# Kernel tuning notes

Hardware: AMD Instinct MI355X
Metric: run time of the kernel (lower is better)

Reference implementation:

```python
import jax, jax.numpy as jnp
import numpy as np

NF = 128                 # num_filters
C_STATE = NF * 3 // 2    # ODE state channels (output of conv_up_embed_1) = 192
EPS = 1e-5               # InstanceNorm2d eps
N_STEPS = 4              # fixed-step RK4 steps over t in [0, 1]
DT = 1.0 / N_STEPS

nl = jax.nn.softplus     # get_nonlinearity('softplus')


def instance_norm(x):
    # InstanceNorm2d(affine=False): normalize over (H, W) per (N, C)
    m = x.mean(axis=(2, 3), keepdims=True)
    v = x.var(axis=(2, 3), keepdims=True)
    return (x - m) * jax.lax.rsqrt(v + EPS)


def conv2d(x, w, b):
    y = jax.lax.conv_general_dilated(
        x, w, window_strides=(1, 1), padding='SAME',
        dimension_numbers=('NCHW', 'OIHW', 'NCHW'))
    return y + b[None, :, None, None]


def setup_inputs() -> dict:
    key = jax.random.key(0)
    ks = jax.random.split(key, 10)
    B, H, W = 4, 64, 64
    s = 0.05
    return {
        'x':    jax.random.normal(ks[0], (B, NF, H, W), jnp.float32),
        'skip': jax.random.normal(ks[1], (B, NF, 2 * H, 2 * W), jnp.float32),
        # InitialVelocity: 3x3 conv nf -> nf
        'iv_w': jax.random.normal(ks[2], (NF, NF, 3, 3), jnp.float32) * s,
        'iv_b': jax.random.normal(ks[3], (NF,), jnp.float32) * s,
        # conv_up_embed_1: 1x1 conv 3nf -> 3nf//2
        'up_w': jax.random.normal(ks[4], (C_STATE, 3 * NF, 1, 1), jnp.float32) * s,
        'up_b': jax.random.normal(ks[5], (C_STATE,), jnp.float32) * s,
        # ConvSODEFunc convs (second-order: dv/dt = f(z, v))
        'f1_w': jax.random.normal(ks[6], (C_STATE // 2, C_STATE, 3, 3), jnp.float32) * s,
        'f1_b': jax.random.normal(ks[7], (C_STATE // 2,), jnp.float32) * s,
        'f2_w': jax.random.normal(ks[8], (C_STATE // 2, C_STATE // 2, 3, 3), jnp.float32) * s,
        'f2_b': jax.random.normal(ks[9], (C_STATE // 2,), jnp.float32) * s,
    }


def _ode_f(y, f1_w, f1_b, f2_w, f2_b):
    # second-order ODE: state y = [z, v]; dz/dt = v, dv/dt = f(y)
    c = y.shape[1] // 2
    v = y[:, c:]
    u = nl(conv2d(instance_norm(y), f1_w, f1_b))   # [B, C/2, H, W]
    dv = nl(conv2d(instance_norm(u), f2_w, f2_b))  # [B, C/2, H, W]
    return jnp.concatenate([v, dv], axis=1)


def reference(x, skip, iv_w, iv_b, up_w, up_b, f1_w, f1_b, f2_w, f2_b):
    # InitialVelocity (counter == 0): concat learned velocity -> 2*nf channels
    v0 = nl(conv2d(instance_norm(x), iv_w, iv_b))
    y = jnp.concatenate([x, v0], axis=1)                       # [B, 2nf, H, W]
    B, C, H, W = y.shape
    # bilinear upsample x2, align_corners=False (half-pixel centers)
    y = jax.image.resize(y, (B, C, 2 * H, 2 * W), method='bilinear')
    y = jnp.concatenate([y, skip], axis=1)                     # [B, 3nf, 2H, 2W]
    y = nl(conv2d(y, up_w, up_b))                              # [B, 3nf//2, 2H, 2W]
    # ODEBlock: integrate t: 0 -> 1, fixed-step RK4 via lax.scan
    f = lambda s: _ode_f(s, f1_w, f1_b, f2_w, f2_b)

    def step(s, _):
        k1 = f(s)
        k2 = f(s + 0.5 * DT * k1)
        k3 = f(s + 0.5 * DT * k2)
        k4 = f(s + DT * k3)
        s = s + (DT / 6.0) * (k1 + 2.0 * k2 + 2.0 * k3 + k4)
        return s, None

    y, _ = jax.lax.scan(step, y, None, length=N_STEPS)
    return y
```

## Files before the change

### kernel.cpp

```cpp
#include <hip/hip_runtime.h>
#include <math.h>

#define BB 4
#define NF 128
#define CS 192
#define CH 96
#define H1 64
#define W1 64
#define H2 128
#define W2 128
#define P1 (H1*W1)
#define P2 (H2*W2)
#define EPSV 1e-5f
#define DTV 0.25f
#define NSLICE 32
#define SLOTSZ (1536 * NSLICE)

typedef __attribute__((ext_vector_type(8))) short short8;
typedef __attribute__((ext_vector_type(4))) float f32x4;

__device__ __forceinline__ float softplus_f(float x) {
    return fmaxf(x, 0.0f) + __logf(1.0f + __expf(-fabsf(x)));
}
__device__ __forceinline__ unsigned f2bf(float f) {
    unsigned u = __float_as_uint(f);
    return (u + 0x7FFFu + ((u >> 16) & 1u)) >> 16;
}
__device__ __forceinline__ float bf2f(short s) {
    return __uint_as_float(((unsigned)(unsigned short)s) << 16);
}
__device__ __forceinline__ int packbf(float a, float b) {
    return (int)(f2bf(a) | (f2bf(b) << 16));
}

__global__ __launch_bounds__(256) void zero_kernel(float* __restrict__ p, int n) {
    int i = blockIdx.x * 256 + threadIdx.x;
    if (i < n) p[i] = 0.f;
}

__global__ __launch_bounds__(256) void meanvar_raw_kernel(const float* __restrict__ x,
                                                          float* __restrict__ mv, int HW) {
    int bc = blockIdx.x;
    const float* p = x + (size_t)bc * HW;
    float s = 0.f, s2 = 0.f;
    for (int i = threadIdx.x; i < HW; i += 256) {
        float v = p[i];
        s += v; s2 += v * v;
    }
    __shared__ float sh[512];
    sh[threadIdx.x] = s; sh[256 + threadIdx.x] = s2;
    __syncthreads();
    for (int o = 128; o > 0; o >>= 1) {
        if (threadIdx.x < o) {
            sh[threadIdx.x] += sh[threadIdx.x + o];
            sh[256 + threadIdx.x] += sh[256 + threadIdx.x + o];
        }
        __syncthreads();
    }
    if (threadIdx.x == 0) {
        mv[2 * bc]     = sh[0];
        mv[2 * bc + 1] = sh[256];
    }
}

__global__ __launch_bounds__(256) void repack_w_kernel(const float* __restrict__ w,
                                                       short* __restrict__ wq,
                                                       int Cout, int Cin) {
    int idx = blockIdx.x * 256 + threadIdx.x;
    int total = Cout * Cin * 9;
    if (idx >= total) return;
    int tap = idx % 9;
    int t = idx / 9;
    int ci = t % Cin, co = t / Cin;
    int NITl = Cin >> 5, COGl = Cout >> 4;
    int cog = co >> 4, lx = co & 15;
    int it = ci >> 5, q = (ci >> 3) & 3, e = ci & 7;
    size_t o = ((((size_t)tap * NITl + it) * COGl + cog) * 64 + q * 16 + lx) * 8 + e;
    wq[o] = (short)f2bf(w[idx]);
}

__global__ __launch_bounds__(256) void repack_w1_kernel(const float* __restrict__ w,
                                                        short* __restrict__ wq,
                                                        int Cout, int Cin) {
    int idx = blockIdx.x * 256 + threadIdx.x;
    if (idx >= Cout * Cin) return;
    int ci = idx % Cin, co = idx / Cin;
    int COGl = Cout >> 4;
    int cog = co >> 4, lx = co & 15;
    int it = ci >> 5, q = (ci >> 3) & 3, e = ci & 7;
    size_t o = (((size_t)it * COGl + cog) * 64 + q * 16 + lx) * 8 + e;
    wq[o] = (short)f2bf(w[idx]);
}

__global__ __launch_bounds__(256) void xcvt_kernel(const float* __restrict__ x,
                                                   short* __restrict__ xbf) {
    __shared__ int buf[64 * 68];
    const int tid = threadIdx.x;
    const int px = tid & 63, jj = tid >> 6;
    const int px0 = blockIdx.x * 64;
    const int b = blockIdx.y;
#pragma unroll
    for (int ji = 0; ji < 16; ji++) {
        int j = jj + 4 * ji;
        int c = 2 * j;
        float a = x[((size_t)(b * NF + c)) * P1 + px0 + px];
        float d = x[((size_t)(b * NF + c + 1)) * P1 + px0 + px];
        buf[px * 68 + j] = packbf(a, d);
    }
    __syncthreads();
#pragma unroll
    for (int k = 0; k < 4; k++) {
        int idx = tid + 256 * k;
        int p2 = idx >> 4, w4 = idx & 15;
        int4 v = *(const int4*)&buf[p2 * 68 + w4 * 4];
        *(int4*)(xbf + ((size_t)b * P1 + px0 + p2) * NF + w4 * 8) = v;
    }
}

template<int CIN, int NCG, bool OUTBF, bool SUMS>
__global__ __launch_bounds__(256) void conv3x3_mfma(
    const short* __restrict__ in, const float* __restrict__ mvsums,
    const short* __restrict__ wq, const float* __restrict__ bias,
    float* __restrict__ outf, short* __restrict__ outbf, float* __restrict__ osum,
    int CoutT, int H, int W, int outC, int outCoff, int coblk)
{
    constexpr int ROWS = CIN + 8;
    constexpr int STGI = 180 * ROWS / 2;
    constexpr int SMEMI = (OUTBF && 128 * 52 > STGI) ? 128 * 52 : STGI;
    constexpr int NCGH = NCG / 2;
    __shared__ int smem[SMEMI];
    short* xt = (short*)smem;
    __shared__ float mvm[CIN], mvr[CIN];
    __shared__ float shs[2 * CH];
    const int tid = threadIdx.x;
    const int w4 = tid >> 6, lane = tid & 63;
    const int wy = w4 & 1, wc = w4 >> 1;
    const int lx = lane & 15, q = lane >> 4;
    const int x0 = blockIdx.x * 16, y0 = blockIdx.y * 8;
    const int b = blockIdx.z / coblk;
    const int co_base = (blockIdx.z % coblk) * (NCG * 16);
    const int slice = (blockIdx.x + (blockIdx.y << 3)) & (NSLICE - 1);
    const int HWp = H * W;
    const short* inb = in + (size_t)b * HWp * CIN;

    const float invHW = 1.0f / (float)HWp;
    for (int c = tid; c < CIN; c += 256) {
        float s = 0.f, s2 = 0.f;
#pragma unroll
        for (int sl = 0; sl < NSLICE; sl++) {
            s  += mvsums[(size_t)sl * 1536 + (b * CIN + c) * 2];
            s2 += mvsums[(size_t)sl * 1536 + (b * CIN + c) * 2 + 1];
        }
        float m  = s * invHW;
        float var = fmaxf(s2 * invHW - m * m, 0.f);
        mvm[c] = m;
        mvr[c] = rsqrtf(var + EPSV);
    }
    if (SUMS) for (int c = tid; c < 2 * CH; c += 256) shs[c] = 0.f;
    __syncthreads();

    constexpr int PARTS = CIN / 8;
    constexpr int TOT = 180 * PARTS;
    constexpr int NJ = (TOT + 255) / 256;
#pragma unroll
    for (int k = 0; k < NJ; k++) {
        int j = tid + 256 * k;
        if (j < TOT) {
            int px = j / PARTS, part = j - px * PARTS;
            int yy = px / 18, xx = px - yy * 18;
            int gy = y0 + yy - 1, gx = x0 + xx - 1;
            int4 wv = make_int4(0, 0, 0, 0);
            if (gy >= 0 && gy < H && gx >= 0 && gx < W) {
                int cb = part * 8;
                short8 v = *(const short8*)(inb + (size_t)(gy * W + gx) * CIN + cb);
                float4 m0 = *(const float4*)&mvm[cb];
                float4 m1 = *(const float4*)&mvm[cb + 4];
                float4 r0 = *(const float4*)&mvr[cb];
                float4 r1 = *(const float4*)&mvr[cb + 4];
                wv.x = packbf((bf2f(v[0]) - m0.x) * r0.x, (bf2f(v[1]) - m0.y) * r0.y);
                wv.y = packbf((bf2f(v[2]) - m0.z) * r0.z, (bf2f(v[3]) - m0.w) * r0.w);
                wv.z = packbf((bf2f(v[4]) - m1.x) * r1.x, (bf2f(v[5]) - m1.y) * r1.y);
                wv.w = packbf((bf2f(v[6]) - m1.z) * r1.z, (bf2f(v[7]) - m1.w) * r1.w);
            }
            *(int4*)(&xt[px * ROWS + part * 8]) = wv;
        }
    }
    __syncthreads();

    f32x4 acc[4][NCGH];
#pragma unroll
    for (int rr = 0; rr < 4; rr++)
#pragma unroll
        for (int cg = 0; cg < NCGH; cg++) acc[rr][cg] = (f32x4)(0.f);

    constexpr int NIT = CIN / 32;
    constexpr int NC = 9 * NIT;
    const int COGl = CoutT >> 4;
    const short* wbase = wq + ((size_t)((co_base >> 4) + wc * NCGH) * 64 + lane) * 8;

    auto ldw = [&](int c, short8* dst) {
        int it = c / 9, tap = c - 9 * it;
        int slot0 = (tap * NIT + it) * COGl;
#pragma unroll
        for (int cg = 0; cg < NCGH; cg++)
            dst[cg] = *(const short8*)(wbase + (size_t)(slot0 + cg) * 512);
    };
    auto body = [&](int c, const short8* a) {
        int it = c / 9, tap = c - 9 * it;
        int dy = tap / 3, dx = tap - 3 * (tap / 3);
        short8 bfr[4];
#pragma unroll
        for (int rr = 0; rr < 4; rr++)
            bfr[rr] = *(const short8*)(
                &xt[((wy * 4 + rr + dy) * 18 + lx + dx) * ROWS + it * 32 + q * 8]);
#pragma unroll
        for (int rr = 0; rr < 4; rr++)
#pragma unroll
            for (int cg = 0; cg < NCGH; cg++)
                acc[rr][cg] = __builtin_amdgcn_mfma_f32_16x16x32_bf16(
                    a[cg], bfr[rr], acc[rr][cg], 0, 0, 0);
    };

    short8 aA[NCGH], aB[NCGH], aC[NCGH];
    ldw(0, aA);
    if (NC > 1) ldw(1, aB);
    for (int c = 0; c < NC; c += 3) {
        if (c + 2 < NC) ldw(c + 2, aC);
        body(c, aA);
        if (c + 3 < NC) ldw(c + 3, aA);
        if (c + 1 < NC) body(c + 1, aB);
        if (c + 4 < NC) ldw(c + 4, aB);
        if (c + 2 < NC) body(c + 2, aC);
    }

    if (OUTBF) __syncthreads();

    float s1l[NCGH][4], s2l[NCGH][4];
    if (SUMS) {
#pragma unroll
        for (int cg = 0; cg < NCGH; cg++)
#pragma unroll
            for (int r = 0; r < 4; r++) { s1l[cg][r] = 0.f; s2l[cg][r] = 0.f; }
    }
#pragma unroll
    for (int rr = 0; rr < 4; rr++) {
        int y = y0 + wy * 4 + rr;
#pragma unroll
        for (int cg = 0; cg < NCGH; cg++) {
            float v[4];
#pragma unroll
            for (int r = 0; r < 4; r++) {
                int co = wc * (NCGH * 16) + cg * 16 + q * 4 + r;
                v[r] = softplus_f(acc[rr][cg][r] + bias[co_base + co]);
                if (SUMS) { s1l[cg][r] += v[r]; s2l[cg][r] += v[r] * v[r]; }
            }
            if (OUTBF) {
                int pl = (wy * 4 + rr) * 16 + lx;
                smem[pl * 52 + wc * (NCGH * 8) + cg * 8 + q * 2]     = packbf(v[0], v[1]);
                smem[pl * 52 + wc * (NCGH * 8) + cg * 8 + q * 2 + 1] = packbf(v[2], v[3]);
            } else {
                float* ob = outf + ((size_t)b * outC + outCoff + co_base) * HWp
                            + y * W + x0 + lx;
#pragma unroll
                for (int r = 0; r < 4; r++)
                    ob[(size_t)(wc * (NCGH * 16) + cg * 16 + q * 4 + r) * HWp] = v[r];
            }
        }
    }
    if (OUTBF) {
        __syncthreads();
#pragma unroll
        for (int k = 0; k < 6; k++) {
            int idx = tid + 256 * k;
            int pl2 = idx / 12, w4i = idx % 12;
            int4 v = *(const int4*)&smem[pl2 * 52 + w4i * 4];
            int pix = (y0 + (pl2 >> 4)) * W + x0 + (pl2 & 15);
            *(int4*)(outbf + ((size_t)b * HWp + pix) * 96 + w4i * 8) = v;
        }
    }
    if (SUMS) {
#pragma unroll
        for (int cg = 0; cg < NCGH; cg++)
#pragma unroll
            for (int r = 0; r < 4; r++) {
                float a1 = s1l[cg][r], a2 = s2l[cg][r];
#pragma unroll
                for (int mask = 1; mask < 16; mask <<= 1) {
                    a1 += __shfl_xor(a1, mask);
                    a2 += __shfl_xor(a2, mask);
                }
                if (lx == 0) {
                    int co = wc * (NCGH * 16) + cg * 16 + q * 4 + r;
                    atomicAdd(&shs[2 * co], a1);
                    atomicAdd(&shs[2 * co + 1], a2);
                }
            }
        __syncthreads();
        for (int c = tid; c < 2 * NCG * 16; c += 256)
            atomicAdd(&osum[(size_t)slice * 1536 + (size_t)b * 2 * NCG * 16 + c], shs[c]);
    }
}

__global__ __launch_bounds__(256) void upsample_kernel(
    const float* __restrict__ x, const float* __restrict__ v0,
    const float* __restrict__ skip, short* __restrict__ ycat)
{
    __shared__ int buf[64 * 98];
    const int tid = threadIdx.x;
    const int px = tid & 63, jj = tid >> 6;
    const int px0 = blockIdx.x * 64;
    const int b = blockIdx.y;
    const int pxg = px0 + px;
    const int ox = pxg & 127, oy = pxg >> 7;
    int my = oy >> 1, mx = ox >> 1;
    int iy0 = (oy & 1) ? my : my - 1;
    float wy0 = (oy & 1) ? 0.75f : 0.25f;
    int ix0 = (ox & 1) ? mx : mx - 1;
    float wx0 = (ox & 1) ? 0.75f : 0.25f;
    int iy1 = min(iy0 + 1, H1 - 1); iy0 = max(iy0, 0);
    int ix1 = min(ix0 + 1, W1 - 1); ix0 = max(ix0, 0);
    float wy1 = 1.f - wy0, wx1 = 1.f - wx0;
    float w00 = wy0 * wx0, w01 = wy0 * wx1, w10 = wy1 * wx0, w11 = wy1 * wx1;
    int o00 = iy0 * W1 + ix0, o01 = iy0 * W1 + ix1;
    int o10 = iy1 * W1 + ix0, o11 = iy1 * W1 + ix1;

#pragma unroll
    for (int half = 0; half < 2; half++) {
        if (half == 1) __syncthreads();
#pragma unroll 4
        for (int ji = 0; ji < 24; ji++) {
            int j = jj + 4 * ji + half * 96;
            int c = 2 * j;
            float a, d;
            if (c < 256) {
                const float* s0 = (c < 128) ? x + ((size_t)(b * NF + c)) * P1
                                            : v0 + ((size_t)(b * NF + c - 128)) * P1;
                const float* s1 = s0 + P1;
                a = w00 * s0[o00] + w01 * s0[o01] + w10 * s0[o10] + w11 * s0[o11];
                d = w00 * s1[o00] + w01 * s1[o01] + w10 * s1[o10] + w11 * s1[o11];
            } else {
                const float* sk = skip + ((size_t)(b * NF + c - 256)) * P2 + pxg;
                a = sk[0]; d = sk[P2];
            }
            buf[px * 98 + (j - half * 96)] = packbf(a, d);
        }
        __syncthreads();
#pragma unroll
        for (int k = 0; k < 6; k++) {
            int idx = tid + 256 * k;
            int p2 = idx / 24, w4 = idx % 24;
            int4 v = *(const int4*)&buf[p2 * 98 + w4 * 4];
            *(int4*)(ycat + ((size_t)b * P2 + px0 + p2) * 384 + half * 192 + w4 * 8) = v;
        }
    }
}

__global__ __launch_bounds__(256) void conv1x1_mfma(
    const short* __restrict__ ycat, const short* __restrict__ wq,
    const float* __restrict__ bias, float* __restrict__ out,
    short* __restrict__ sbf, float* __restrict__ osum)
{
    __shared__ int smem[64 * 196];
    short* xs = (short*)smem;
    const int tid = threadIdx.x;
    const int wave = tid >> 6, lane = tid & 63;
    const int lx = lane & 15, q = lane >> 4;
    const int p0 = blockIdx.x * 64;
    const int b = blockIdx.y;
    const int slice = blockIdx.x & (NSLICE - 1);

    const short* yb = ycat + ((size_t)b * P2 + p0) * 384;
#pragma unroll
    for (int k = 0; k < 12; k++) {
        int j = tid + 256 * k;
        int spx = j / 48, spart = j - spx * 48;
        short8 v = *(const short8*)(yb + (size_t)spx * 384 + spart * 8);
        *(short8*)(&xs[spx * 392 + spart * 8]) = v;
    }
    __syncthreads();

    f32x4 acc[3][4];
#pragma unroll
    for (int cg = 0; cg < 3; cg++)
#pragma unroll
        for (int pg = 0; pg < 4; pg++) acc[cg][pg] = (f32x4)(0.f);

    const short* wbase = wq + ((size_t)(wave * 3) * 64 + lane) * 8;
    auto ldw = [&](int it, short8* dst) {
#pragma unroll
        for (int cg = 0; cg < 3; cg++)
            dst[cg] = *(const short8*)(wbase + (size_t)(it * 12 + cg) * 512);
    };
    auto body = [&](int it, const short8* a) {
        short8 bfr[4];
#pragma unroll
        for (int pg = 0; pg < 4; pg++)
            bfr[pg] = *(const short8*)(&xs[(pg * 16 + lx) * 392 + it * 32 + q * 8]);
#pragma unroll
        for (int pg = 0; pg < 4; pg++)
#pragma unroll
            for (int cg = 0; cg < 3; cg++)
                acc[cg][pg] = __builtin_amdgcn_mfma_f32_16x16x32_bf16(
                    a[cg], bfr[pg], acc[cg][pg], 0, 0, 0);
    };

    short8 aA[3], aB[3], aC[3];
    ldw(0, aA);
    ldw(1, aB);
    for (int c = 0; c < 12; c += 3) {
        if (c + 2 < 12) ldw(c + 2, aC);
        body(c, aA);
        if (c + 3 < 12) ldw(c + 3, aA);
        body(c + 1, aB);
        if (c + 4 < 12) ldw(c + 4, aB);
        if (c + 2 < 12) body(c + 2, aC);
    }
    __syncthreads();

    float s1a[3][4], s2a[3][4];
#pragma unroll
    for (int cg = 0; cg < 3; cg++)
#pragma unroll
        for (int r = 0; r < 4; r++) { s1a[cg][r] = 0.f; s2a[cg][r] = 0.f; }
#pragma unroll
    for (int cg = 0; cg < 3; cg++) {
        int co0 = wave * 48 + cg * 16 + q * 4;
#pragma unroll
        for (int pg = 0; pg < 4; pg++) {
            int pl = pg * 16 + lx;
            float v[4];
#pragma unroll
            for (int r = 0; r < 4; r++) {
                v[r] = softplus_f(acc[cg][pg][r] + bias[co0 + r]);
                out[((size_t)(b * CS + co0 + r)) * P2 + p0 + pl] = v[r];
                s1a[cg][r] += v[r]; s2a[cg][r] += v[r] * v[r];
            }
            smem[pl * 100 + (co0 >> 1)]     = packbf(v[0], v[1]);
            smem[pl * 100 + (co0 >> 1) + 1] = packbf(v[2], v[3]);
        }
    }
    __syncthreads();
#pragma unroll
    for (int k = 0; k < 6; k++) {
        int idx = tid + 256 * k;
        int p2 = idx / 24, w4 = idx % 24;
        int4 v = *(const int4*)&smem[p2 * 100 + w4 * 4];
        *(int4*)(sbf + ((size_t)b * P2 + p0 + p2) * 192 + w4 * 8) = v;
    }
#pragma unroll
    for (int cg = 0; cg < 3; cg++)
#pragma unroll
        for (int r = 0; r < 4; r++) {
            float a1 = s1a[cg][r], a2 = s2a[cg][r];
#pragma unroll
            for (int mask = 1; mask < 16; mask <<= 1) {
                a1 += __shfl_xor(a1, mask);
                a2 += __shfl_xor(a2, mask);
            }
            if (lx == 0) {
                int co = wave * 48 + cg * 16 + q * 4 + r;
                atomicAdd(&osum[(size_t)slice * 1536 + ((size_t)b * CS + co) * 2], a1);
                atomicAdd(&osum[(size_t)slice * 1536 + ((size_t)b * CS + co) * 2 + 1], a2);
            }
        }
}

__global__ __launch_bounds__(256) void combine_kernel(
    const float* __restrict__ S, const float* __restrict__ Gx,
    const float* __restrict__ Gp, short* __restrict__ T, float* __restrict__ osum,
    float ca1, float ca2, float cb)
{
    __shared__ int buf[64 * 100];
    const int tid = threadIdx.x;
    const int px = tid & 63, jj = tid >> 6;
    const int px0 = blockIdx.x * 64;
    const int b = blockIdx.y;
    const int pxg = px0 + px;
    const int slice = blockIdx.x & (NSLICE - 1);
#pragma unroll 3
    for (int ji = 0; ji < 12; ji++) {
        int j = jj + 4 * ji;
        int c = 2 * j;
        size_t ia = ((size_t)(b * CS + c)) * P2 + pxg;
        size_t ib = ia + (size_t)CH * P2;
        size_t ig = ((size_t)(b * CH + c)) * P2 + pxg;
        float sa0 = S[ia], sa1 = S[ia + P2];
        float sb0 = S[ib], sb1 = S[ib + P2];
        float gx0 = Gx[ig], gx1 = Gx[ig + P2];
        float gp0 = Gp[ig], gp1 = Gp[ig + P2];
        buf[px * 100 + j]      = packbf(sa0 + ca1 * sb0 + ca2 * gx0,
                                        sa1 + ca1 * sb1 + ca2 * gx1);
        buf[px * 100 + 48 + j] = packbf(sb0 + cb * gp0, sb1 + cb * gp1);
    }
    __syncthreads();
#pragma unroll
    for (int k = 0; k < 6; k++) {
        int idx = tid + 256 * k;
        int p2 = idx / 24, w4 = idx % 24;
        int4 v = *(const int4*)&buf[p2 * 100 + w4 * 4];
        *(int4*)(T + ((size_t)b * P2 + px0 + p2) * 192 + w4 * 8) = v;
    }
    if (tid < 192) {
        int jj2 = tid >> 1, s = tid & 1;
        float s1lo = 0.f, s2lo = 0.f, s1hi = 0.f, s2hi = 0.f;
#pragma unroll 8
        for (int p = s; p < 64; p += 2) {
            int v = buf[p * 100 + jj2];
            float lo = bf2f((short)v), hi = bf2f((short)(v >> 16));
            s1lo += lo; s2lo += lo * lo; s1hi += hi; s2hi += hi * hi;
        }
        s1lo += __shfl_xor(s1lo, 1); s2lo += __shfl_xor(s2lo, 1);
        s1hi += __shfl_xor(s1hi, 1); s2hi += __shfl_xor(s2hi, 1);
        if (s == 0) {
            int c = 2 * jj2;
            float* dst = &osum[(size_t)slice * 1536 + ((size_t)b * CS + c) * 2];
            atomicAdd(dst, s1lo);
            atomicAdd(dst + 1, s2lo);
            atomicAdd(dst + 2, s1hi);
            atomicAdd(dst + 3, s2hi);
        }
    }
}

template<bool SBF>
__global__ __launch_bounds__(256) void final_kernel(
    float* __restrict__ S, const float* __restrict__ G1, const float* __restrict__ G2,
    const float* __restrict__ G3, const float* __restrict__ G4,
    short* __restrict__ sbf, float* __restrict__ osum)
{
    __shared__ int buf[SBF ? 64 * 100 : 4];
    const int tid = threadIdx.x;
    const int px = tid & 63, jj = tid >> 6;
    const int px0 = blockIdx.x * 64;
    const int b = blockIdx.y;
    const int pxg = px0 + px;
    const int slice = blockIdx.x & (NSLICE - 1);
    const float cA = DTV * DTV / 6.0f, cB = DTV / 6.0f;
#pragma unroll 3
    for (int ji = 0; ji < 12; ji++) {
        int j = jj + 4 * ji;
        int c = 2 * j;
        size_t ia = ((size_t)(b * CS + c)) * P2 + pxg;
        size_t ib = ia + (size_t)CH * P2;
        size_t ig = ((size_t)(b * CH + c)) * P2 + pxg;
        float sa0 = S[ia], sa1 = S[ia + P2];
        float sb0 = S[ib], sb1 = S[ib + P2];
        float g10 = G1[ig], g11 = G1[ig + P2];
        float g20 = G2[ig], g21 = G2[ig + P2];
        float g30 = G3[ig], g31 = G3[ig + P2];
        float g40 = G4[ig], g41 = G4[ig + P2];
        float na0 = sa0 + DTV * sb0 + cA * (g10 + g20 + g30);
        float na1 = sa1 + DTV * sb1 + cA * (g11 + g21 + g31);
        float nb0 = sb0 + cB * (g10 + 2.f * g20 + 2.f * g30 + g40);
        float nb1 = sb1 + cB * (g11 + 2.f * g21 + 2.f * g31 + g41);
        S[ia] = na0; S[ia + P2] = na1;
        S[ib] = nb0; S[ib + P2] = nb1;
        if (SBF) {
            buf[px * 100 + j]      = packbf(na0, na1);
            buf[px * 100 + 48 + j] = packbf(nb0, nb1);
        }
    }
    if (SBF) {
        __syncthreads();
#pragma unroll
        for (int k = 0; k < 6; k++) {
            int idx = tid + 256 * k;
            int p2 = idx / 24, w4 = idx % 24;
            int4 v = *(const int4*)&buf[p2 * 100 + w4 * 4];
            *(int4*)(sbf + ((size_t)b * P2 + px0 + p2) * 192 + w4 * 8) = v;
        }
        if (tid < 192) {
            int jj2 = tid >> 1, s = tid & 1;
            float s1lo = 0.f, s2lo = 0.f, s1hi = 0.f, s2hi = 0.f;
#pragma unroll 8
            for (int p = s; p < 64; p += 2) {
                int v = buf[p * 100 + jj2];
                float lo = bf2f((short)v), hi = bf2f((short)(v >> 16));
                s1lo += lo; s2lo += lo * lo; s1hi += hi; s2hi += hi * hi;
            }
            s1lo += __shfl_xor(s1lo, 1); s2lo += __shfl_xor(s2lo, 1);
            s1hi += __shfl_xor(s1hi, 1); s2hi += __shfl_xor(s2hi, 1);
            if (s == 0) {
                int c = 2 * jj2;
                float* dst = &osum[(size_t)slice * 1536 + ((size_t)b * CS + c) * 2];
                atomicAdd(dst, s1lo);
                atomicAdd(dst + 1, s2lo);
                atomicAdd(dst + 2, s1hi);
                atomicAdd(dst + 3, s2hi);
            }
        }
    }
}

extern "C" void kernel_launch(void* const* d_in, const int* in_sizes, int n_in,
                              void* d_out, int out_size, void* d_ws, size_t ws_size,
                              hipStream_t stream) {
    (void)in_sizes; (void)n_in; (void)out_size; (void)ws_size;
    const float* x    = (const float*)d_in[0];
    const float* skip = (const float*)d_in[1];
    const float* iv_w = (const float*)d_in[2];
    const float* iv_b = (const float*)d_in[3];
    const float* up_w = (const float*)d_in[4];
    const float* up_b = (const float*)d_in[5];
    const float* f1_w = (const float*)d_in[6];
    const float* f1_b = (const float*)d_in[7];
    const float* f2_w = (const float*)d_in[8];
    const float* f2_b = (const float*)d_in[9];

    float* S = (float*)d_out;
    float* ws = (float*)d_ws;
    const size_t NGf = (size_t)BB * CH * P2;
    float* G1 = ws;
    float* G2 = G1 + NGf;
    float* G3 = G2 + NGf;
    float* G4 = G3 + NGf;
    short* T   = (short*)(G4 + NGf);
    short* U   = T + (size_t)BB * P2 * CS;
    short* SBF = U + (size_t)BB * P2 * CH;
    float* MVS = (float*)(SBF + (size_t)BB * P2 * CS);
    short* IVQ = (short*)(MVS + (size_t)34 * SLOTSZ);
    short* F1Q = IVQ + (size_t)9 * NF * NF;
    short* F2Q = F1Q + (size_t)9 * CH * CS;
    short* UPQ = F2Q + (size_t)9 * CH * CH;
    short* YCAT = (short*)G1;
    float* V0   = G3;
    short* XBF  = (short*)G4;

    auto slot = [&](int i) { return MVS + (size_t)i * SLOTSZ; };

    zero_kernel<<<(34 * SLOTSZ + 255) / 256, 256, 0, stream>>>(MVS, 34 * SLOTSZ);
    repack_w_kernel<<<(NF * NF * 9 + 255) / 256, 256, 0, stream>>>(iv_w, IVQ, NF, NF);
    repack_w_kernel<<<(CH * CS * 9 + 255) / 256, 256, 0, stream>>>(f1_w, F1Q, CH, CS);
    repack_w_kernel<<<(CH * CH * 9 + 255) / 256, 256, 0, stream>>>(f2_w, F2Q, CH, CH);
    repack_w1_kernel<<<(CS * 384 + 255) / 256, 256, 0, stream>>>(up_w, UPQ, CS, 384);

    meanvar_raw_kernel<<<BB * NF, 256, 0, stream>>>(x, slot(0), P1);
    xcvt_kernel<<<dim3(P1 / 64, BB), 256, 0, stream>>>(x, XBF);
    conv3x3_mfma<128, 4, false, false><<<dim3(W1 / 16, H1 / 8, BB * 2), 256, 0, stream>>>(
        XBF, slot(0), IVQ, iv_b, V0, nullptr, nullptr, NF, H1, W1, NF, 0, 2);
    upsample_kernel<<<dim3(P2 / 64, BB), 256, 0, stream>>>(x, V0, skip, YCAT);
    conv1x1_mfma<<<dim3(P2 / 64, BB), 256, 0, stream>>>(YCAT, UPQ, up_b, S, SBF, slot(1));

    const float h = DTV;
    float* G[4] = {G1, G2, G3, G4};
    int sc = 2;
    float* yslot = slot(1);
    const dim3 egrd(P2 / 64, BB);

    for (int step = 0; step < 4; step++) {
        for (int sub = 0; sub < 4; sub++) {
            const short* Ybf = (sub == 0) ? SBF : T;
            float* uslot = slot(sc++);
            conv3x3_mfma<192, 6, true, true><<<dim3(W2 / 16, H2 / 8, BB), 256, 0, stream>>>(
                Ybf, yslot, F1Q, f1_b, nullptr, U, uslot, CH, H2, W2, CH, 0, 1);
            conv3x3_mfma<96, 6, false, false><<<dim3(W2 / 16, H2 / 8, BB), 256, 0, stream>>>(
                U, uslot, F2Q, f2_b, G[sub], nullptr, nullptr, CH, H2, W2, CH, 0, 1);
            if (sub < 3) {
                float ca1, ca2, cb;
                const float *Gx, *Gp;
                if (sub == 0)      { ca1 = h/2; ca2 = 0.f;     Gx = G1; Gp = G1; cb = h/2; }
                else if (sub == 1) { ca1 = h/2; ca2 = h*h/4;   Gx = G1; Gp = G2; cb = h/2; }
                else               { ca1 = h;   ca2 = h*h/2;   Gx = G2; Gp = G3; cb = h;   }
                float* tslot = slot(sc++);
                combine_kernel<<<egrd, 256, 0, stream>>>(S, Gx, Gp, T, tslot, ca1, ca2, cb);
                yslot = tslot;
            }
        }
        if (step < 3) {
            float* sslot = slot(sc++);
            final_kernel<true><<<egrd, 256, 0, stream>>>(S, G1, G2, G3, G4, SBF, sslot);
            yslot = sslot;
        } else {
            final_kernel<false><<<egrd, 256, 0, stream>>>(S, G1, G2, G3, G4, SBF, nullptr);
        }
    }
}
```

Measured before the change: 1.519 ms.

## Use 512-thread conv blocks with K-split staging and fuse upsample into 1x1 conv

The 3x3 conv kernels move from four to eight waves per block. Each wave now covers two output rows instead of four, which roughly halves the accumulator registers. The 192-channel conv stages its input tile in two channel halves so the LDS footprint shrinks, at the cost of an extra sync and a second staging pass. Separately, the bilinear upsample is fused into the 1x1 conv kernel, which removes the YCAT intermediate round-trip through global memory.

```diff
diff --git a/kernel.cpp b/kernel.cpp
--- a/kernel.cpp
+++ b/kernel.cpp
@@ -117,14 +117,15 @@
     }
 }
 
-template<int CIN, int NCG, bool OUTBF, bool SUMS>
-__global__ __launch_bounds__(256) void conv3x3_mfma(
+template<int CIN, int KS, int NCG, bool OUTBF, bool SUMS>
+__global__ __launch_bounds__(512, 4) void conv3x3_mfma(
     const short* __restrict__ in, const float* __restrict__ mvsums,
     const short* __restrict__ wq, const float* __restrict__ bias,
     float* __restrict__ outf, short* __restrict__ outbf, float* __restrict__ osum,
     int CoutT, int H, int W, int outC, int outCoff, int coblk)
 {
-    constexpr int ROWS = CIN + 8;
+    constexpr int CINH = CIN / KS;
+    constexpr int ROWS = CINH + 8;
     constexpr int STGI = 180 * ROWS / 2;
     constexpr int SMEMI = (OUTBF && 128 * 52 > STGI) ? 128 * 52 : STGI;
     constexpr int NCGH = NCG / 2;
@@ -133,8 +134,8 @@
     __shared__ float mvm[CIN], mvr[CIN];
     __shared__ float shs[2 * CH];
     const int tid = threadIdx.x;
-    const int w4 = tid >> 6, lane = tid & 63;
-    const int wy = w4 & 1, wc = w4 >> 1;
+    const int w8 = tid >> 6, lane = tid & 63;
+    const int wy = w8 & 3, wc = w8 >> 2;
     const int lx = lane & 15, q = lane >> 4;
     const int x0 = blockIdx.x * 16, y0 = blockIdx.y * 8;
     const int b = blockIdx.z / coblk;
@@ -144,7 +145,7 @@
     const short* inb = in + (size_t)b * HWp * CIN;
 
     const float invHW = 1.0f / (float)HWp;
-    for (int c = tid; c < CIN; c += 256) {
+    for (int c = tid; c < CIN; c += 512) {
         float s = 0.f, s2 = 0.f;
 #pragma unroll
         for (int sl = 0; sl < NSLICE; sl++) {
@@ -156,81 +157,85 @@
         mvm[c] = m;
         mvr[c] = rsqrtf(var + EPSV);
     }
-    if (SUMS) for (int c = tid; c < 2 * CH; c += 256) shs[c] = 0.f;
+    if (SUMS) for (int c = tid; c < 2 * CH; c += 512) shs[c] = 0.f;
     __syncthreads();
 
-    constexpr int PARTS = CIN / 8;
+    constexpr int PARTS = CINH / 8;
     constexpr int TOT = 180 * PARTS;
-    constexpr int NJ = (TOT + 255) / 256;
-#pragma unroll
-    for (int k = 0; k < NJ; k++) {
-        int j = tid + 256 * k;
-        if (j < TOT) {
-            int px = j / PARTS, part = j - px * PARTS;
-            int yy = px / 18, xx = px - yy * 18;
-            int gy = y0 + yy - 1, gx = x0 + xx - 1;
-            int4 wv = make_int4(0, 0, 0, 0);
-            if (gy >= 0 && gy < H && gx >= 0 && gx < W) {
-                int cb = part * 8;
-                short8 v = *(const short8*)(inb + (size_t)(gy * W + gx) * CIN + cb);
-                float4 m0 = *(const float4*)&mvm[cb];
-                float4 m1 = *(const float4*)&mvm[cb + 4];
-                float4 r0 = *(const float4*)&mvr[cb];
-                float4 r1 = *(const float4*)&mvr[cb + 4];
-                wv.x = packbf((bf2f(v[0]) - m0.x) * r0.x, (bf2f(v[1]) - m0.y) * r0.y);
-                wv.y = packbf((bf2f(v[2]) - m0.z) * r0.z, (bf2f(v[3]) - m0.w) * r0.w);
-                wv.z = packbf((bf2f(v[4]) - m1.x) * r1.x, (bf2f(v[5]) - m1.y) * r1.y);
-                wv.w = packbf((bf2f(v[6]) - m1.z) * r1.z, (bf2f(v[7]) - m1.w) * r1.w);
-            }
-            *(int4*)(&xt[px * ROWS + part * 8]) = wv;
-        }
-    }
-    __syncthreads();
-
-    f32x4 acc[4][NCGH];
-#pragma unroll
-    for (int rr = 0; rr < 4; rr++)
-#pragma unroll
-        for (int cg = 0; cg < NCGH; cg++) acc[rr][cg] = (f32x4)(0.f);
-
+    constexpr int NJ = (TOT + 511) / 512;
     constexpr int NIT = CIN / 32;
-    constexpr int NC = 9 * NIT;
+    constexpr int NITH = CINH / 32;
+    constexpr int NC = 9 * NITH;
     const int COGl = CoutT >> 4;
     const short* wbase = wq + ((size_t)((co_base >> 4) + wc * NCGH) * 64 + lane) * 8;
 
-    auto ldw = [&](int c, short8* dst) {
-        int it = c / 9, tap = c - 9 * it;
-        int slot0 = (tap * NIT + it) * COGl;
-#pragma unroll
-        for (int cg = 0; cg < NCGH; cg++)
-            dst[cg] = *(const short8*)(wbase + (size_t)(slot0 + cg) * 512);
-    };
-    auto body = [&](int c, const short8* a) {
-        int it = c / 9, tap = c - 9 * it;
-        int dy = tap / 3, dx = tap - 3 * (tap / 3);
-        short8 bfr[4];
-#pragma unroll
-        for (int rr = 0; rr < 4; rr++)
-            bfr[rr] = *(const short8*)(
-                &xt[((wy * 4 + rr + dy) * 18 + lx + dx) * ROWS + it * 32 + q * 8]);
-#pragma unroll
-        for (int rr = 0; rr < 4; rr++)
+    f32x4 acc[2][NCGH];
+#pragma unroll
+    for (int rr = 0; rr < 2; rr++)
+#pragma unroll
+        for (int cg = 0; cg < NCGH; cg++) acc[rr][cg] = (f32x4)(0.f);
+
+    for (int p = 0; p < KS; p++) {
+        if (p > 0) __syncthreads();
+#pragma unroll
+        for (int k = 0; k < NJ; k++) {
+            int j = tid + 512 * k;
+            if (j < TOT) {
+                int px = j / PARTS, part = j - px * PARTS;
+                int yy = px / 18, xx = px - yy * 18;
+                int gy = y0 + yy - 1, gx = x0 + xx - 1;
+                int4 wv = make_int4(0, 0, 0, 0);
+                if (gy >= 0 && gy < H && gx >= 0 && gx < W) {
+                    int cb = p * CINH + part * 8;
+                    short8 v = *(const short8*)(inb + (size_t)(gy * W + gx) * CIN + cb);
+                    float4 m0 = *(const float4*)&mvm[cb];
+                    float4 m1 = *(const float4*)&mvm[cb + 4];
+                    float4 r0 = *(const float4*)&mvr[cb];
+                    float4 r1 = *(const float4*)&mvr[cb + 4];
+                    wv.x = packbf((bf2f(v[0]) - m0.x) * r0.x, (bf2f(v[1]) - m0.y) * r0.y);
+                    wv.y = packbf((bf2f(v[2]) - m0.z) * r0.z, (bf2f(v[3]) - m0.w) * r0.w);
+                    wv.z = packbf((bf2f(v[4]) - m1.x) * r1.x, (bf2f(v[5]) - m1.y) * r1.y);
+                    wv.w = packbf((bf2f(v[6]) - m1.z) * r1.z, (bf2f(v[7]) - m1.w) * r1.w);
+                }
+                *(int4*)(&xt[px * ROWS + part * 8]) = wv;
+            }
+        }
+        __syncthreads();
+
+        auto ldw = [&](int c, short8* dst) {
+            int itl = c / 9, tap = c - 9 * itl;
+            int slot0 = (tap * NIT + p * NITH + itl) * COGl;
 #pragma unroll
             for (int cg = 0; cg < NCGH; cg++)
-                acc[rr][cg] = __builtin_amdgcn_mfma_f32_16x16x32_bf16(
-                    a[cg], bfr[rr], acc[rr][cg], 0, 0, 0);
-    };
-
-    short8 aA[NCGH], aB[NCGH], aC[NCGH];
-    ldw(0, aA);
-    if (NC > 1) ldw(1, aB);
-    for (int c = 0; c < NC; c += 3) {
-        if (c + 2 < NC) ldw(c + 2, aC);
-        body(c, aA);
-        if (c + 3 < NC) ldw(c + 3, aA);
-        if (c + 1 < NC) body(c + 1, aB);
-        if (c + 4 < NC) ldw(c + 4, aB);
-        if (c + 2 < NC) body(c + 2, aC);
+                dst[cg] = *(const short8*)(wbase + (size_t)(slot0 + cg) * 512);
+        };
+        auto body = [&](int c, const short8* a) {
+            int itl = c / 9, tap = c - 9 * itl;
+            int dy = tap / 3, dx = tap - 3 * (tap / 3);
+            short8 bfr[2];
+#pragma unroll
+            for (int rr = 0; rr < 2; rr++)
+                bfr[rr] = *(const short8*)(
+                    &xt[((wy * 2 + rr + dy) * 18 + lx + dx) * ROWS + itl * 32 + q * 8]);
+#pragma unroll
+            for (int rr = 0; rr < 2; rr++)
+#pragma unroll
+                for (int cg = 0; cg < NCGH; cg++)
+                    acc[rr][cg] = __builtin_amdgcn_mfma_f32_16x16x32_bf16(
+                        a[cg], bfr[rr], acc[rr][cg], 0, 0, 0);
+        };
+
+        short8 aA[NCGH], aB[NCGH], aC[NCGH];
+        ldw(0, aA);
+        ldw(1, aB);
+        for (int c = 0; c < NC; c += 3) {
+            if (c + 2 < NC) ldw(c + 2, aC);
+            body(c, aA);
+            if (c + 3 < NC) ldw(c + 3, aA);
+            if (c + 1 < NC) body(c + 1, aB);
+            if (c + 4 < NC) ldw(c + 4, aB);
+            if (c + 2 < NC) body(c + 2, aC);
+        }
     }
 
     if (OUTBF) __syncthreads();
@@ -243,8 +248,8 @@
             for (int r = 0; r < 4; r++) { s1l[cg][r] = 0.f; s2l[cg][r] = 0.f; }
     }
 #pragma unroll
-    for (int rr = 0; rr < 4; rr++) {
-        int y = y0 + wy * 4 + rr;
+    for (int rr = 0; rr < 2; rr++) {
+        int y = y0 + wy * 2 + rr;
 #pragma unroll
         for (int cg = 0; cg < NCGH; cg++) {
             float v[4];
@@ -255,7 +260,7 @@
                 if (SUMS) { s1l[cg][r] += v[r]; s2l[cg][r] += v[r] * v[r]; }
             }
             if (OUTBF) {
-                int pl = (wy * 4 + rr) * 16 + lx;
+                int pl = (wy * 2 + rr) * 16 + lx;
                 smem[pl * 52 + wc * (NCGH * 8) + cg * 8 + q * 2]     = packbf(v[0], v[1]);
                 smem[pl * 52 + wc * (NCGH * 8) + cg * 8 + q * 2 + 1] = packbf(v[2], v[3]);
             } else {
@@ -270,8 +275,8 @@
     if (OUTBF) {
         __syncthreads();
 #pragma unroll
-        for (int k = 0; k < 6; k++) {
-            int idx = tid + 256 * k;
+        for (int k = 0; k < 3; k++) {
+            int idx = tid + 512 * k;
             int pl2 = idx / 12, w4i = idx % 12;
             int4 v = *(const int4*)&smem[pl2 * 52 + w4i * 4];
             int pix = (y0 + (pl2 >> 4)) * W + x0 + (pl2 & 15);
@@ -296,21 +301,28 @@
                 }
             }
         __syncthreads();
-        for (int c = tid; c < 2 * NCG * 16; c += 256)
+        for (int c = tid; c < 2 * NCG * 16; c += 512)
             atomicAdd(&osum[(size_t)slice * 1536 + (size_t)b * 2 * NCG * 16 + c], shs[c]);
     }
 }
 
-__global__ __launch_bounds__(256) void upsample_kernel(
+__global__ __launch_bounds__(256, 3) void upconv1x1_mfma(
     const float* __restrict__ x, const float* __restrict__ v0,
-    const float* __restrict__ skip, short* __restrict__ ycat)
+    const float* __restrict__ skip, const short* __restrict__ wq,
+    const float* __restrict__ bias, float* __restrict__ out,
+    short* __restrict__ sbf, float* __restrict__ osum)
 {
-    __shared__ int buf[64 * 98];
+    __shared__ int smem[64 * 196];
+    short* xs = (short*)smem;
     const int tid = threadIdx.x;
+    const int wave = tid >> 6, lane = tid & 63;
+    const int lx = lane & 15, q = lane >> 4;
+    const int p0 = blockIdx.x * 64;
+    const int b = blockIdx.y;
+    const int slice = blockIdx.x & (NSLICE - 1);
+
     const int px = tid & 63, jj = tid >> 6;
-    const int px0 = blockIdx.x * 64;
-    const int b = blockIdx.y;
-    const int pxg = px0 + px;
+    const int pxg = p0 + px;
     const int ox = pxg & 127, oy = pxg >> 7;
     int my = oy >> 1, mx = ox >> 1;
     int iy0 = (oy & 1) ? my : my - 1;
@@ -323,59 +335,22 @@
     float w00 = wy0 * wx0, w01 = wy0 * wx1, w10 = wy1 * wx0, w11 = wy1 * wx1;
     int o00 = iy0 * W1 + ix0, o01 = iy0 * W1 + ix1;
     int o10 = iy1 * W1 + ix0, o11 = iy1 * W1 + ix1;
-
-#pragma unroll
-    for (int half = 0; half < 2; half++) {
-        if (half == 1) __syncthreads();
 #pragma unroll 4
-        for (int ji = 0; ji < 24; ji++) {
-            int j = jj + 4 * ji + half * 96;
-            int c = 2 * j;
-            float a, d;
-            if (c < 256) {
-                const float* s0 = (c < 128) ? x + ((size_t)(b * NF + c)) * P1
-                                            : v0 + ((size_t)(b * NF + c - 128)) * P1;
-                const float* s1 = s0 + P1;
-                a = w00 * s0[o00] + w01 * s0[o01] + w10 * s0[o10] + w11 * s0[o11];
-                d = w00 * s1[o00] + w01 * s1[o01] + w10 * s1[o10] + w11 * s1[o11];
-            } else {
-                const float* sk = skip + ((size_t)(b * NF + c - 256)) * P2 + pxg;
-                a = sk[0]; d = sk[P2];
-            }
-            buf[px * 98 + (j - half * 96)] = packbf(a, d);
-        }
-        __syncthreads();
-#pragma unroll
-        for (int k = 0; k < 6; k++) {
-            int idx = tid + 256 * k;
-            int p2 = idx / 24, w4 = idx % 24;
-            int4 v = *(const int4*)&buf[p2 * 98 + w4 * 4];
-            *(int4*)(ycat + ((size_t)b * P2 + px0 + p2) * 384 + half * 192 + w4 * 8) = v;
-        }
-    }
-}
-
-__global__ __launch_bounds__(256) void conv1x1_mfma(
-    const short* __restrict__ ycat, const short* __restrict__ wq,
-    const float* __restrict__ bias, float* __restrict__ out,
-    short* __restrict__ sbf, float* __restrict__ osum)
-{
-    __shared__ int smem[64 * 196];
-    short* xs = (short*)smem;
-    const int tid = threadIdx.x;
-    const int wave = tid >> 6, lane = tid & 63;
-    const int lx = lane & 15, q = lane >> 4;
-    const int p0 = blockIdx.x * 64;
-    const int b = blockIdx.y;
-    const int slice = blockIdx.x & (NSLICE - 1);
-
-    const short* yb = ycat + ((size_t)b * P2 + p0) * 384;
-#pragma unroll
-    for (int k = 0; k < 12; k++) {
-        int j = tid + 256 * k;
-        int spx = j / 48, spart = j - spx * 48;
-        short8 v = *(const short8*)(yb + (size_t)spx * 384 + spart * 8);
-        *(short8*)(&xs[spx * 392 + spart * 8]) = v;
+    for (int ji = 0; ji < 48; ji++) {
+        int j = jj + 4 * ji;
+        int c = 2 * j;
+        float a, d;
+        if (c < 256) {
+            const float* s0 = (c < 128) ? x + ((size_t)(b * NF + c)) * P1
+                                        : v0 + ((size_t)(b * NF + c - 128)) * P1;
+            const float* s1 = s0 + P1;
+            a = w00 * s0[o00] + w01 * s0[o01] + w10 * s0[o10] + w11 * s0[o11];
+            d = w00 * s1[o00] + w01 * s1[o01] + w10 * s1[o10] + w11 * s1[o11];
+        } else {
+            const float* sk = skip + ((size_t)(b * NF + c - 256)) * P2 + pxg;
+            a = sk[0]; d = sk[P2];
+        }
+        smem[px * 196 + j] = packbf(a, d);
     }
     __syncthreads();
 
@@ -622,7 +597,6 @@
     short* F1Q = IVQ + (size_t)9 * NF * NF;
     short* F2Q = F1Q + (size_t)9 * CH * CS;
     short* UPQ = F2Q + (size_t)9 * CH * CH;
-    short* YCAT = (short*)G1;
     float* V0   = G3;
     short* XBF  = (short*)G4;
 
@@ -636,10 +610,10 @@
 
     meanvar_raw_kernel<<<BB * NF, 256, 0, stream>>>(x, slot(0), P1);
     xcvt_kernel<<<dim3(P1 / 64, BB), 256, 0, stream>>>(x, XBF);
-    conv3x3_mfma<128, 4, false, false><<<dim3(W1 / 16, H1 / 8, BB * 2), 256, 0, stream>>>(
+    conv3x3_mfma<128, 1, 4, false, false><<<dim3(W1 / 16, H1 / 8, BB * 2), 512, 0, stream>>>(
         XBF, slot(0), IVQ, iv_b, V0, nullptr, nullptr, NF, H1, W1, NF, 0, 2);
-    upsample_kernel<<<dim3(P2 / 64, BB), 256, 0, stream>>>(x, V0, skip, YCAT);
-    conv1x1_mfma<<<dim3(P2 / 64, BB), 256, 0, stream>>>(YCAT, UPQ, up_b, S, SBF, slot(1));
+    upconv1x1_mfma<<<dim3(P2 / 64, BB), 256, 0, stream>>>(
+        x, V0, skip, UPQ, up_b, S, SBF, slot(1));
 
     const float h = DTV;
     float* G[4] = {G1, G2, G3, G4};
@@ -651,9 +625,9 @@
         for (int sub = 0; sub < 4; sub++) {
             const short* Ybf = (sub == 0) ? SBF : T;
             float* uslot = slot(sc++);
-            conv3x3_mfma<192, 6, true, true><<<dim3(W2 / 16, H2 / 8, BB), 256, 0, stream>>>(
+            conv3x3_mfma<192, 2, 6, true, true><<<dim3(W2 / 16, H2 / 8, BB), 512, 0, stream>>>(
                 Ybf, yslot, F1Q, f1_b, nullptr, U, uslot, CH, H2, W2, CH, 0, 1);
-            conv3x3_mfma<96, 6, false, false><<<dim3(W2 / 16, H2 / 8, BB), 256, 0, stream>>>(
+            conv3x3_mfma<96, 1, 6, false, false><<<dim3(W2 / 16, H2 / 8, BB), 512, 0, stream>>>(
                 U, uslot, F2Q, f2_b, G[sub], nullptr, nullptr, CH, H2, W2, CH, 0, 1);
             if (sub < 3) {
                 float ca1, ca2, cb;
```

Measured after the change: 1.567 ms. 3.1% more time.

## Fuse bilinear upsample and concat into the 1x1 conv MFMA kernel

Applied to the files above, without the earlier changes.

The upsample kernel and the 1x1 conv kernel become one kernel, removing the bf16 YCAT intermediate written to and read back from global memory. Each block builds half of the 384 input channels for its 64 pixels in shared memory, runs the MFMA K-loop over that half, then reuses the buffer for the second half. This halves the shared-memory footprint and lets launch_bounds ask for 5 blocks per SM, at the cost of an extra barrier and less overlap between loading and MFMA work within a block.

```diff
diff --git a/kernel.cpp b/kernel.cpp
--- a/kernel.cpp
+++ b/kernel.cpp
@@ -301,16 +301,23 @@
     }
 }
 
-__global__ __launch_bounds__(256) void upsample_kernel(
+__global__ __launch_bounds__(256, 5) void upconv1x1_mfma(
     const float* __restrict__ x, const float* __restrict__ v0,
-    const float* __restrict__ skip, short* __restrict__ ycat)
+    const float* __restrict__ skip, const short* __restrict__ wq,
+    const float* __restrict__ bias, float* __restrict__ out,
+    short* __restrict__ sbf, float* __restrict__ osum)
 {
-    __shared__ int buf[64 * 98];
+    __shared__ int smem[64 * 100];
+    short* xs = (short*)smem;
     const int tid = threadIdx.x;
+    const int wave = tid >> 6, lane = tid & 63;
+    const int lx = lane & 15, q = lane >> 4;
+    const int p0 = blockIdx.x * 64;
+    const int b = blockIdx.y;
+    const int slice = blockIdx.x & (NSLICE - 1);
+
     const int px = tid & 63, jj = tid >> 6;
-    const int px0 = blockIdx.x * 64;
-    const int b = blockIdx.y;
-    const int pxg = px0 + px;
+    const int pxg = p0 + px;
     const int ox = pxg & 127, oy = pxg >> 7;
     int my = oy >> 1, mx = ox >> 1;
     int iy0 = (oy & 1) ? my : my - 1;
@@ -323,6 +330,31 @@
     float w00 = wy0 * wx0, w01 = wy0 * wx1, w10 = wy1 * wx0, w11 = wy1 * wx1;
     int o00 = iy0 * W1 + ix0, o01 = iy0 * W1 + ix1;
     int o10 = iy1 * W1 + ix0, o11 = iy1 * W1 + ix1;
+
+    f32x4 acc[3][4];
+#pragma unroll
+    for (int cg = 0; cg < 3; cg++)
+#pragma unroll
+        for (int pg = 0; pg < 4; pg++) acc[cg][pg] = (f32x4)(0.f);
+
+    const short* wbase = wq + ((size_t)(wave * 3) * 64 + lane) * 8;
+    auto ldw = [&](int it, short8* dst) {
+#pragma unroll
+        for (int cg = 0; cg < 3; cg++)
+            dst[cg] = *(const short8*)(wbase + (size_t)(it * 12 + cg) * 512);
+    };
+    auto mbody = [&](int itl, const short8* a) {
+        short8 bfr[4];
+#pragma unroll
+        for (int pg = 0; pg < 4; pg++)
+            bfr[pg] = *(const short8*)(&xs[(pg * 16 + lx) * 200 + itl * 32 + q * 8]);
+#pragma unroll
+        for (int pg = 0; pg < 4; pg++)
+#pragma unroll
+            for (int cg = 0; cg < 3; cg++)
+                acc[cg][pg] = __builtin_amdgcn_mfma_f32_16x16x32_bf16(
+                    a[cg], bfr[pg], acc[cg][pg], 0, 0, 0);
+    };
 
 #pragma unroll
     for (int half = 0; half < 2; half++) {
@@ -342,78 +374,22 @@
                 const float* sk = skip + ((size_t)(b * NF + c - 256)) * P2 + pxg;
                 a = sk[0]; d = sk[P2];
             }
-            buf[px * 98 + (j - half * 96)] = packbf(a, d);
+            smem[px * 100 + (j - half * 96)] = packbf(a, d);
         }
         __syncthreads();
-#pragma unroll
-        for (int k = 0; k < 6; k++) {
-            int idx = tid + 256 * k;
-            int p2 = idx / 24, w4 = idx % 24;
-            int4 v = *(const int4*)&buf[p2 * 98 + w4 * 4];
-            *(int4*)(ycat + ((size_t)b * P2 + px0 + p2) * 384 + half * 192 + w4 * 8) = v;
-        }
-    }
-}
-
-__global__ __launch_bounds__(256) void conv1x1_mfma(
-    const short* __restrict__ ycat, const short* __restrict__ wq,
-    const float* __restrict__ bias, float* __restrict__ out,
-    short* __restrict__ sbf, float* __restrict__ osum)
-{
-    __shared__ int smem[64 * 196];
-    short* xs = (short*)smem;
-    const int tid = threadIdx.x;
-    const int wave = tid >> 6, lane = tid & 63;
-    const int lx = lane & 15, q = lane >> 4;
-    const int p0 = blockIdx.x * 64;
-    const int b = blockIdx.y;
-    const int slice = blockIdx.x & (NSLICE - 1);
-
-    const short* yb = ycat + ((size_t)b * P2 + p0) * 384;
-#pragma unroll
-    for (int k = 0; k < 12; k++) {
-        int j = tid + 256 * k;
-        int spx = j / 48, spart = j - spx * 48;
-        short8 v = *(const short8*)(yb + (size_t)spx * 384 + spart * 8);
-        *(short8*)(&xs[spx * 392 + spart * 8]) = v;
-    }
-    __syncthreads();
-
-    f32x4 acc[3][4];
-#pragma unroll
-    for (int cg = 0; cg < 3; cg++)
-#pragma unroll
-        for (int pg = 0; pg < 4; pg++) acc[cg][pg] = (f32x4)(0.f);
-
-    const short* wbase = wq + ((size_t)(wave * 3) * 64 + lane) * 8;
-    auto ldw = [&](int it, short8* dst) {
-#pragma unroll
-        for (int cg = 0; cg < 3; cg++)
-            dst[cg] = *(const short8*)(wbase + (size_t)(it * 12 + cg) * 512);
-    };
-    auto body = [&](int it, const short8* a) {
-        short8 bfr[4];
-#pragma unroll
-        for (int pg = 0; pg < 4; pg++)
-            bfr[pg] = *(const short8*)(&xs[(pg * 16 + lx) * 392 + it * 32 + q * 8]);
-#pragma unroll
-        for (int pg = 0; pg < 4; pg++)
-#pragma unroll
-            for (int cg = 0; cg < 3; cg++)
-                acc[cg][pg] = __builtin_amdgcn_mfma_f32_16x16x32_bf16(
-                    a[cg], bfr[pg], acc[cg][pg], 0, 0, 0);
-    };
-
-    short8 aA[3], aB[3], aC[3];
-    ldw(0, aA);
-    ldw(1, aB);
-    for (int c = 0; c < 12; c += 3) {
-        if (c + 2 < 12) ldw(c + 2, aC);
-        body(c, aA);
-        if (c + 3 < 12) ldw(c + 3, aA);
-        body(c + 1, aB);
-        if (c + 4 < 12) ldw(c + 4, aB);
-        if (c + 2 < 12) body(c + 2, aC);
+
+        short8 aA[3], aB[3], aC[3];
+        ldw(half * 6 + 0, aA);
+        ldw(half * 6 + 1, aB);
+#pragma unroll
+        for (int c = 0; c < 6; c += 3) {
+            ldw(half * 6 + c + 2, aC);
+            mbody(c, aA);
+            if (c + 3 < 6) ldw(half * 6 + c + 3, aA);
+            mbody(c + 1, aB);
+            if (c + 4 < 6) ldw(half * 6 + c + 4, aB);
+            mbody(c + 2, aC);
+        }
     }
     __syncthreads();
 
@@ -622,7 +598,6 @@
     short* F1Q = IVQ + (size_t)9 * NF * NF;
     short* F2Q = F1Q + (size_t)9 * CH * CS;
     short* UPQ = F2Q + (size_t)9 * CH * CH;
-    short* YCAT = (short*)G1;
     float* V0   = G3;
     short* XBF  = (short*)G4;
 
@@ -638,8 +613,8 @@
     xcvt_kernel<<<dim3(P1 / 64, BB), 256, 0, stream>>>(x, XBF);
     conv3x3_mfma<128, 4, false, false><<<dim3(W1 / 16, H1 / 8, BB * 2), 256, 0, stream>>>(
         XBF, slot(0), IVQ, iv_b, V0, nullptr, nullptr, NF, H1, W1, NF, 0, 2);
-    upsample_kernel<<<dim3(P2 / 64, BB), 256, 0, stream>>>(x, V0, skip, YCAT);
-    conv1x1_mfma<<<dim3(P2 / 64, BB), 256, 0, stream>>>(YCAT, UPQ, up_b, S, SBF, slot(1));
+    upconv1x1_mfma<<<dim3(P2 / 64, BB), 256, 0, stream>>>(
+        x, V0, skip, UPQ, up_b, S, SBF, slot(1));
 
     const float h = DTV;
     float* G[4] = {G1, G2, G3, G4};
```

Result: slower. 1.682 ms (+10.7%).
